# Kernel optimization log

Measured on AMD Instinct MI355X. Metric: run time of the kernel, lower is better.

The kernel has to match this reference:

```python
import jax, jax.numpy as jnp
import numpy as np

D_MODEL = 1280
N_HEADS = 16
DEPTH = D_MODEL // N_HEADS  # 80
NEG_BIG = -10000.0


def setup_inputs() -> dict:
    key = jax.random.key(0)
    ks = jax.random.split(key, 12)
    B, S = 2, 2048
    std = 1.0 / np.sqrt(D_MODEL)
    inp = {
        "v": jax.random.normal(ks[0], (B, S, D_MODEL), jnp.float32),
        "k": jax.random.normal(ks[1], (B, S, D_MODEL), jnp.float32),
        "q": jax.random.normal(ks[2], (B, S, D_MODEL), jnp.float32),
        # causal mask: 1.0 on strictly-upper triangle (future positions)
        "mask": jnp.triu(jnp.ones((S, S), jnp.float32), k=1),
        "Wq_w": jax.random.normal(ks[3], (D_MODEL, D_MODEL), jnp.float32) * std,
        "Wq_b": jnp.zeros((D_MODEL,), jnp.float32),
        "Wk_w": jax.random.normal(ks[4], (D_MODEL, D_MODEL), jnp.float32) * std,
        "Wk_b": jnp.zeros((D_MODEL,), jnp.float32),
        "Wv_w": jax.random.normal(ks[5], (D_MODEL, D_MODEL), jnp.float32) * std,
        "Wv_b": jnp.zeros((D_MODEL,), jnp.float32),
        "dense_w": jax.random.normal(ks[6], (D_MODEL, D_MODEL), jnp.float32) * std,
        "dense_b": jnp.zeros((D_MODEL,), jnp.float32),
    }
    return inp


def _split_heads(x, B):
    # [B, S, D] -> [B, H, S, depth]
    return x.reshape(B, -1, N_HEADS, DEPTH).transpose(0, 2, 1, 3)


def reference(v, k, q, mask, Wq_w, Wq_b, Wk_w, Wk_b, Wv_w, Wv_b, dense_w, dense_b):
    B = q.shape[0]
    # torch Linear: y = x @ W.T + b
    qh = _split_heads(q @ Wq_w.T + Wq_b, B)
    kh = _split_heads(k @ Wk_w.T + Wk_b, B)
    vh = _split_heads(v @ Wv_w.T + Wv_b, B)

    scale = 1.0 / np.sqrt(DEPTH)
    logits = jnp.einsum("bhqd,bhkd->bhqk", qh, kh) * scale  # [B,H,S,S]
    nd, ns = logits.shape[-2], logits.shape[-1]
    logits = logits + mask[ns - nd:ns, :ns] * NEG_BIG
    attn = jax.nn.softmax(logits, axis=-1)
    out = jnp.einsum("bhqk,bhkd->bhqd", attn, vh)  # [B,H,S,depth]
    out = out.transpose(0, 2, 1, 3).reshape(B, -1, D_MODEL)
    out = out @ dense_w.T + dense_b
    return out, attn
```

## Files before the change

### kernel.cpp

```cpp
#include <hip/hip_runtime.h>
#include <hip/hip_bf16.h>

typedef short frag8 __attribute__((ext_vector_type(8)));
typedef float facc4 __attribute__((ext_vector_type(4)));
typedef float f32x4 __attribute__((ext_vector_type(4)));
typedef unsigned short ushort_t;
typedef unsigned int uint_t;

#define DEV static __device__ __forceinline__

DEV ushort_t f2bf(float f) {
  uint_t u = __float_as_uint(f);
  u += 0x7fffu + ((u >> 16) & 1u);
  return (ushort_t)(u >> 16);
}
DEV uint_t cvt_pk(float lo, float hi) {
  uint_t r;
  asm("v_cvt_pk_bf16_f32 %0, %1, %2" : "=v"(r) : "v"(lo), "v"(hi));
  return r;
}
DEV frag8 pack8(float4 a, float4 b) {
  union { frag8 f; uint4 u; } u_;
  u_.u.x = cvt_pk(a.x, a.y); u_.u.y = cvt_pk(a.z, a.w);
  u_.u.z = cvt_pk(b.x, b.y); u_.u.w = cvt_pk(b.z, b.w);
  return u_.f;
}
DEV void bar_lds() { asm volatile("s_waitcnt lgkmcnt(0)\n\ts_barrier" ::: "memory"); }

constexpr int B_ = 2, S_ = 2048, H_ = 16, DM = 1280, DH = 80, DP = 96;
constexpr size_t IN_E = (size_t)B_ * S_ * DM;
constexpr size_t WT_E = (size_t)DM * DM;
constexpr size_t OFF_WQ = 0;
constexpr size_t OFF_WK = OFF_WQ + WT_E;
constexpr size_t OFF_WV = OFF_WK + WT_E;
constexpr size_t OFF_WD = OFF_WV + WT_E;
constexpr size_t QH_E  = (size_t)B_ * H_ * S_ * DP;
constexpr size_t OFF_QH = OFF_WD + WT_E;
constexpr size_t OFF_KH = OFF_QH + QH_E;
constexpr size_t VT_E  = (size_t)B_ * H_ * DH * S_;
constexpr size_t OFF_VT = OFF_KH + QH_E;
constexpr size_t OFF_OH = OFF_VT + VT_E;

constexpr float QSCALE = 0.16129822f;

__global__ void convert_kernel(const float* __restrict__ wq, const float* __restrict__ wk,
                               const float* __restrict__ wv, const float* __restrict__ wd,
                               ushort_t* __restrict__ ws) {
  size_t i = (size_t)blockIdx.x * blockDim.x + threadIdx.x;
  size_t stride = (size_t)gridDim.x * blockDim.x;
  constexpr size_t TOTAL = 4 * WT_E / 8;
  constexpr size_t NROW = (size_t)B_ * H_ * S_;
  constexpr size_t PADC = 2 * NROW * 2;
  for (size_t c = i; c < TOTAL + PADC; c += stride) {
    if (c < TOTAL) {
      size_t e = c * 8;
      const float* s2; size_t lo;
      if      (e < WT_E)     { s2 = wq; lo = e; }
      else if (e < 2 * WT_E) { s2 = wk; lo = e - WT_E; }
      else if (e < 3 * WT_E) { s2 = wv; lo = e - 2 * WT_E; }
      else                   { s2 = wd; lo = e - 3 * WT_E; }
      float4 a = *(const float4*)(s2 + lo);
      float4 b = *(const float4*)(s2 + lo + 4);
      uint4 o;
      o.x = (uint_t)f2bf(a.x) | ((uint_t)f2bf(a.y) << 16);
      o.y = (uint_t)f2bf(a.z) | ((uint_t)f2bf(a.w) << 16);
      o.z = (uint_t)f2bf(b.x) | ((uint_t)f2bf(b.y) << 16);
      o.w = (uint_t)f2bf(b.z) | ((uint_t)f2bf(b.w) << 16);
      *(uint4*)(ws + e) = o;
    } else {
      size_t rr = c - TOTAL;
      size_t row = rr >> 1;
      size_t base = (row < NROW ? OFF_QH : OFF_KH) + (row & (NROW - 1)) * DP + DH + (rr & 1) * 8;
      uint4 z = {0u, 0u, 0u, 0u};
      *(uint4*)(ws + base) = z;
    }
  }
}

__global__ __launch_bounds__(256) void qkv_kernel(const float* __restrict__ Aq,
                                                  const float* __restrict__ Ak,
                                                  const float* __restrict__ Av,
                                                  const ushort_t* __restrict__ wts,
                                                  const float* __restrict__ bq,
                                                  const float* __restrict__ bk,
                                                  const float* __restrict__ bv,
                                                  ushort_t* __restrict__ qh_o,
                                                  ushort_t* __restrict__ kh_o,
                                                  ushort_t* __restrict__ vt_o) {
  __shared__ __align__(16) ushort_t sA[2][128][40];
  __shared__ __align__(16) ushort_t sB[2][128][40];
  int which = blockIdx.x / 320;
  int local = blockIdx.x - which * 320;
  int swz = (local & 7) * 40 + (local >> 3);
  int tm = swz / 10, tn = swz % 10;
  int m0 = tm * 128, n0 = tn * 128;
  const float* A = which == 0 ? Aq : which == 1 ? Ak : Av;
  const ushort_t* W = wts + (size_t)which * WT_E;
  const float* bias = which == 0 ? bq : which == 1 ? bk : bv;
  int tid = threadIdx.x, l = tid & 63, wv = tid >> 6;
  int lm = l & 15, lg = l >> 4;
  int wr = wv >> 1, wc = wv & 1;
  int srow = tid >> 2, schk = tid & 3;
  facc4 acc[4][4] = {};
  frag8 ra[2], rb[2];

  auto load_tile = [&](int kt) {
    const float* Ab = A + (size_t)(m0 + srow) * DM + kt * 32 + schk * 8;
    ra[0] = pack8(*(const float4*)Ab, *(const float4*)(Ab + 4));
    const float* Ab2 = Ab + (size_t)64 * DM;
    ra[1] = pack8(*(const float4*)Ab2, *(const float4*)(Ab2 + 4));
    const ushort_t* Bb = W + (size_t)(n0 + srow) * DM + kt * 32 + schk * 8;
    rb[0] = *(const frag8*)Bb;
    rb[1] = *(const frag8*)(Bb + (size_t)64 * DM);
  };
  auto store_tile = [&](int bb) {
    *(frag8*)&sA[bb][srow][schk * 8] = ra[0];
    *(frag8*)&sA[bb][srow + 64][schk * 8] = ra[1];
    *(frag8*)&sB[bb][srow][schk * 8] = rb[0];
    *(frag8*)&sB[bb][srow + 64][schk * 8] = rb[1];
  };

  load_tile(0);
  store_tile(0);
  __syncthreads();
  for (int kt = 0; kt < 40; ++kt) {
    int cur = kt & 1;
    if (kt < 39) load_tile(kt + 1);
    frag8 af[4], bf[4];
#pragma unroll
    for (int i = 0; i < 4; ++i) af[i] = *(const frag8*)&sA[cur][wr * 64 + i * 16 + lm][lg * 8];
#pragma unroll
    for (int i = 0; i < 4; ++i) bf[i] = *(const frag8*)&sB[cur][wc * 64 + i * 16 + lm][lg * 8];
#pragma unroll
    for (int mi = 0; mi < 4; ++mi)
#pragma unroll
      for (int ni = 0; ni < 4; ++ni)
        acc[mi][ni] = __builtin_amdgcn_mfma_f32_16x16x32_bf16(af[mi], bf[ni], acc[mi][ni], 0, 0, 0);
    if (kt < 39) store_tile(cur ^ 1);
    __syncthreads();
  }

  float scale = (which == 0) ? QSCALE : 1.0f;
  ushort_t* dst = which == 0 ? qh_o : which == 1 ? kh_o : vt_o;
#pragma unroll
  for (int ni = 0; ni < 4; ++ni) {
    int n = n0 + wc * 64 + ni * 16 + lm;
    float bv2 = bias[n];
    int h = n / 80, d = n % 80;
#pragma unroll
    for (int mi = 0; mi < 4; ++mi) {
      int mbase = m0 + wr * 64 + mi * 16 + lg * 4;
      int b = mbase >> 11, sp = mbase & 2047;
      if (which < 2) {
#pragma unroll
        for (int r = 0; r < 4; ++r) {
          float vl = (acc[mi][ni][r] + bv2) * scale;
          dst[((size_t)(b * H_ + h) * S_ + sp + r) * DP + d] = f2bf(vl);
        }
      } else {
        uint2 u2;
        u2.x = cvt_pk(acc[mi][ni][0] + bv2, acc[mi][ni][1] + bv2);
        u2.y = cvt_pk(acc[mi][ni][2] + bv2, acc[mi][ni][3] + bv2);
        *(uint2*)&dst[((size_t)(b * H_ + h) * DH + d) * S_ + sp] = u2;
      }
    }
  }
}

__global__ __launch_bounds__(256) void dense_kernel(const ushort_t* __restrict__ A,
                                                    const ushort_t* __restrict__ W,
                                                    const float* __restrict__ bias,
                                                    float* __restrict__ dst_f) {
  __shared__ __align__(16) ushort_t sA[2][128][40];
  __shared__ __align__(16) ushort_t sB[2][128][40];
  int bid = blockIdx.x;
  int swz = (bid & 7) * 40 + (bid >> 3);
  int tm = swz / 10, tn = swz % 10;
  int m0 = tm * 128, n0 = tn * 128;
  int tid = threadIdx.x, l = tid & 63, wv = tid >> 6;
  int lm = l & 15, lg = l >> 4;
  int wr = wv >> 1, wc = wv & 1;
  int srow = tid >> 2, schk = tid & 3;
  facc4 acc[4][4] = {};
  frag8 ra[2], rb[2];

  auto load_tile = [&](int kt) {
    const ushort_t* Ab = A + (size_t)(m0 + srow) * DM + kt * 32 + schk * 8;
    ra[0] = *(const frag8*)Ab;
    ra[1] = *(const frag8*)(Ab + (size_t)64 * DM);
    const ushort_t* Bb = W + (size_t)(n0 + srow) * DM + kt * 32 + schk * 8;
    rb[0] = *(const frag8*)Bb;
    rb[1] = *(const frag8*)(Bb + (size_t)64 * DM);
  };
  auto store_tile = [&](int bb) {
    *(frag8*)&sA[bb][srow][schk * 8] = ra[0];
    *(frag8*)&sA[bb][srow + 64][schk * 8] = ra[1];
    *(frag8*)&sB[bb][srow][schk * 8] = rb[0];
    *(frag8*)&sB[bb][srow + 64][schk * 8] = rb[1];
  };

  load_tile(0);
  store_tile(0);
  __syncthreads();
  for (int kt = 0; kt < 40; ++kt) {
    int cur = kt & 1;
    if (kt < 39) load_tile(kt + 1);
    frag8 af[4], bf[4];
#pragma unroll
    for (int i = 0; i < 4; ++i) af[i] = *(const frag8*)&sA[cur][wr * 64 + i * 16 + lm][lg * 8];
#pragma unroll
    for (int i = 0; i < 4; ++i) bf[i] = *(const frag8*)&sB[cur][wc * 64 + i * 16 + lm][lg * 8];
#pragma unroll
    for (int mi = 0; mi < 4; ++mi)
#pragma unroll
      for (int ni = 0; ni < 4; ++ni)
        acc[mi][ni] = __builtin_amdgcn_mfma_f32_16x16x32_bf16(af[mi], bf[ni], acc[mi][ni], 0, 0, 0);
    if (kt < 39) store_tile(cur ^ 1);
    __syncthreads();
  }

#pragma unroll
  for (int ni = 0; ni < 4; ++ni) {
    int n = n0 + wc * 64 + ni * 16 + lm;
    float bv2 = bias[n];
#pragma unroll
    for (int mi = 0; mi < 4; ++mi) {
      int mbase = m0 + wr * 64 + mi * 16 + lg * 4;
#pragma unroll
      for (int r = 0; r < 4; ++r)
        __builtin_nontemporal_store(acc[mi][ni][r] + bv2, dst_f + (size_t)(mbase + r) * DM + n);
    }
  }
}

__global__ __launch_bounds__(512, 4) void attn_kernel(const ushort_t* __restrict__ qh,
                                                      const ushort_t* __restrict__ kh,
                                                      const ushort_t* __restrict__ vt,
                                                      ushort_t* __restrict__ outh,
                                                      float* __restrict__ out_attn) {
  __shared__ __align__(16) ushort_t sK[2][64][104];
  __shared__ __align__(16) ushort_t sV[2][80][68];
  __shared__ __align__(16) char sP[8 * 2048];
  int bid = blockIdx.x;
  int half = bid >> 8, rr0 = bid & 255;
  int swz = (rr0 & 7) * 32 + (rr0 >> 3);
  int bh = swz >> 3, pr = swz & 7;
  int b = bh >> 4, h = bh & 15;
  int s = half ? (15 - pr) : pr;
  int tid = threadIdx.x, w = tid >> 6, l = tid & 63, lm = l & 15, lg = l >> 4;
  const ushort_t* qhb = qh + (size_t)bh * S_ * DP;
  const ushort_t* khb = kh + (size_t)bh * S_ * DP;
  const ushort_t* vtb = vt + (size_t)bh * DH * S_;
  float* attnb = out_attn + (size_t)bh * S_ * S_;
  char* Pw = sP + w * 2048;

  int sr[3], sc[3];
#pragma unroll
  for (int i = 0; i < 3; ++i) {
    int c = tid * 3 + i;
    sr[i] = c / 24; sc[i] = (c % 24) * 4;
  }
  uint2 stk[3];
  auto ldtK = [&](int t) {
#pragma unroll
    for (int i = 0; i < 3; ++i)
      stk[i] = *(const uint2*)(khb + (size_t)(t * 64 + sr[i]) * DP + sc[i]);
  };
  auto sttK = [&](int bb) {
#pragma unroll
    for (int i = 0; i < 3; ++i)
      *(uint2*)&sK[bb][sr[i]][sc[i]] = stk[i];
  };
  int vrow = tid >> 3, vcol = (tid & 7) * 8;
  uint4 stv0, stv1;
  auto ldtV = [&](int t) {
    stv0 = *(const uint4*)(vtb + (size_t)vrow * S_ + t * 64 + vcol);
    if (tid < 128) stv1 = *(const uint4*)(vtb + (size_t)(64 + vrow) * S_ + t * 64 + vcol);
  };
  auto sttV = [&](int bb) {
    *(uint4*)&sV[bb][vrow][vcol] = stv0;
    if (tid < 128) *(uint4*)&sV[bb][64 + vrow][vcol] = stv1;
  };

  int q0 = s * 128;
  int wq0 = q0 + w * 16;
  int qg = wq0 + lm;

  frag8 qf[3];
#pragma unroll
  for (int kd = 0; kd < 3; ++kd)
    qf[kd] = *(const frag8*)(qhb + (size_t)qg * DP + kd * 32 + lg * 8);
  int NT = 2 * (s + 1);

  float rs4[4] = {0.f, 0.f, 0.f, 0.f};
  ldtK(0); sttK(0);
  if (NT > 1) ldtK(1);
  bar_lds();
  for (int t = 0; t < NT; ++t) {
    int cur = t & 1;
    if (t + 1 < NT) sttK(cur ^ 1);
    if (t + 2 < NT) ldtK(t + 2);
    if (64 * t < wq0 + 16) {
      facc4 acc[4] = {};
#pragma unroll
      for (int mi = 0; mi < 4; ++mi)
#pragma unroll
        for (int kd = 0; kd < 3; ++kd) {
          frag8 af = *(const frag8*)((const char*)sK + cur * (64 * 104 * 2) +
                                     (mi * 16 + lm) * 208 + kd * 64 + lg * 16);
          acc[mi] = __builtin_amdgcn_mfma_f32_16x16x32_bf16(af, qf[kd], acc[mi], 0, 0, 0);
        }
      if (64 * t + 63 <= wq0) {
#pragma unroll
        for (int mi = 0; mi < 4; ++mi)
#pragma unroll
          for (int r = 0; r < 4; ++r) rs4[r] += exp2f(acc[mi][r]);
      } else {
#pragma unroll
        for (int mi = 0; mi < 4; ++mi)
#pragma unroll
          for (int r = 0; r < 4; ++r) {
            int kg = t * 64 + mi * 16 + lg * 4 + r;
            if (kg <= qg) rs4[r] += exp2f(acc[mi][r]);
          }
      }
    }
    bar_lds();
  }
  float rs = (rs4[0] + rs4[1]) + (rs4[2] + rs4[3]);
  rs += __shfl_xor(rs, 16);
  rs += __shfl_xor(rs, 32);
  float li = -__log2f(rs);

  facc4 acc2[5] = {};
  ldtK(0); ldtV(0); sttK(0); sttV(0);
  if (NT > 1) { ldtK(1); ldtV(1); }
  bar_lds();
  for (int t = 0; t < NT; ++t) {
    int cur = t & 1;
    if (t + 1 < NT) { sttK(cur ^ 1); sttV(cur ^ 1); }
    if (t + 2 < NT) { ldtK(t + 2); ldtV(t + 2); }
    if (64 * t >= wq0 + 16) {
      f32x4 z = {0.f, 0.f, 0.f, 0.f};
#pragma unroll
      for (int mi = 0; mi < 4; ++mi)
        *(f32x4*)(attnb + (size_t)qg * S_ + t * 64 + mi * 16 + lg * 4) = z;
    } else {
      facc4 acc[4] = {};
#pragma unroll
      for (int mi = 0; mi < 4; ++mi)
#pragma unroll
        for (int kd = 0; kd < 3; ++kd) {
          frag8 af = *(const frag8*)((const char*)sK + cur * (64 * 104 * 2) +
                                     (mi * 16 + lm) * 208 + kd * 64 + lg * 16);
          acc[mi] = __builtin_amdgcn_mfma_f32_16x16x32_bf16(af, qf[kd], acc[mi], 0, 0, 0);
        }
      bool full = (64 * t + 63 <= wq0);
#pragma unroll
      for (int mi = 0; mi < 4; ++mi) {
        float p[4];
        if (full) {
#pragma unroll
          for (int r = 0; r < 4; ++r) p[r] = exp2f(acc[mi][r] + li);
        } else {
#pragma unroll
          for (int r = 0; r < 4; ++r) {
            int kg = t * 64 + mi * 16 + lg * 4 + r;
            p[r] = (kg <= qg) ? exp2f(acc[mi][r] + li) : 0.f;
          }
        }
        f32x4 f4 = {p[0], p[1], p[2], p[3]};
        *(f32x4*)(attnb + (size_t)qg * S_ + t * 64 + mi * 16 + lg * 4) = f4;
        uint2 pk;
        pk.x = cvt_pk(p[0], p[1]);
        pk.y = cvt_pk(p[2], p[3]);
        int kb = mi * 32 + lg * 8;
        *(uint2*)(Pw + lm * 128 + (kb ^ ((lm & 7) << 4))) = pk;
      }
#pragma unroll
      for (int ks = 0; ks < 2; ++ks) {
        int kbyte = ks * 64 + lg * 16;
        frag8 pa = *(const frag8*)(Pw + lm * 128 + (kbyte ^ ((lm & 7) << 4)));
#pragma unroll
        for (int nf = 0; nf < 5; ++nf) {
          frag8 vb = *(const frag8*)&sV[cur][nf * 16 + lm][ks * 32 + lg * 8];
          acc2[nf] = __builtin_amdgcn_mfma_f32_16x16x32_bf16(pa, vb, acc2[nf], 0, 0, 0);
        }
      }
    }
    bar_lds();
  }
#pragma unroll
  for (int nf = 0; nf < 5; ++nf)
#pragma unroll
    for (int r = 0; r < 4; ++r) {
      int qrow = q0 + w * 16 + lg * 4 + r;
      int col = h * DH + nf * 16 + lm;
      outh[((size_t)b * S_ + qrow) * DM + col] = f2bf(acc2[nf][r]);
    }

  if (s < 15) {
    int c0 = (s + 1) * 128;
    int r2 = tid >> 2;
    int l4 = (tid & 3) << 2;
    float* rowp = attnb + (size_t)(q0 + r2) * S_ + c0 + l4;
    f32x4 z = {0.f, 0.f, 0.f, 0.f};
    for (int cc = 0; cc < 2048 - c0; cc += 16)
      __builtin_nontemporal_store(z, (f32x4*)(rowp + cc));
  }
}

extern "C" void kernel_launch(void* const* d_in, const int* in_sizes, int n_in,
                              void* d_out, int out_size, void* d_ws, size_t ws_size,
                              hipStream_t stream) {
  const float* v  = (const float*)d_in[0];
  const float* k  = (const float*)d_in[1];
  const float* q  = (const float*)d_in[2];
  const float* wq = (const float*)d_in[4];
  const float* bq = (const float*)d_in[5];
  const float* wk = (const float*)d_in[6];
  const float* bk = (const float*)d_in[7];
  const float* wv = (const float*)d_in[8];
  const float* bv = (const float*)d_in[9];
  const float* wd = (const float*)d_in[10];
  const float* bd = (const float*)d_in[11];
  ushort_t* ws = (ushort_t*)d_ws;
  float* out  = (float*)d_out;
  float* attn = out + IN_E;

  convert_kernel<<<2048, 256, 0, stream>>>(wq, wk, wv, wd, ws);
  qkv_kernel<<<960, 256, 0, stream>>>(q, k, v, ws + OFF_WQ, bq, bk, bv,
                                      ws + OFF_QH, ws + OFF_KH, ws + OFF_VT);
  attn_kernel<<<512, 512, 0, stream>>>(ws + OFF_QH, ws + OFF_KH, ws + OFF_VT, ws + OFF_OH, attn);
  dense_kernel<<<320, 256, 0, stream>>>(ws + OFF_OH, ws + OFF_WD, bd, out);
}
```

Before: 318.9 us.

## Split softmax row-sum pass into separate kernel parallelized over key halves

Moves the first attention pass, which computes the softmax denominators, out of attn_kernel into a new sweep1_kernel. That kernel splits each query block's key range into two halves across twice as many blocks, has a lighter LDS footprint allowing higher occupancy, and combines the partial sums with atomicAdd into a zeroed workspace buffer. attn_kernel then reads the precomputed sums and runs only the second pass. The aim is better parallelism and occupancy for the row-sum pass. The cost is an extra launch, a workspace zeroing step, atomics, and reading K twice across kernels.

New measurement: 347.0 us. 8.8% more time.

```diff
diff --git a/kernel.cpp b/kernel.cpp
--- a/kernel.cpp
+++ b/kernel.cpp
@@ -40,6 +40,7 @@
 constexpr size_t VT_E  = (size_t)B_ * H_ * DH * S_;
 constexpr size_t OFF_VT = OFF_KH + QH_E;
 constexpr size_t OFF_OH = OFF_VT + VT_E;
+constexpr size_t OFF_LS = OFF_OH + IN_E;
 
 constexpr float QSCALE = 0.16129822f;
 
@@ -51,7 +52,8 @@
   constexpr size_t TOTAL = 4 * WT_E / 8;
   constexpr size_t NROW = (size_t)B_ * H_ * S_;
   constexpr size_t PADC = 2 * NROW * 2;
-  for (size_t c = i; c < TOTAL + PADC; c += stride) {
+  constexpr size_t LSC  = 131072 / 8;
+  for (size_t c = i; c < TOTAL + PADC + LSC; c += stride) {
     if (c < TOTAL) {
       size_t e = c * 8;
       const float* s2; size_t lo;
@@ -67,12 +69,16 @@
       o.z = (uint_t)f2bf(b.x) | ((uint_t)f2bf(b.y) << 16);
       o.w = (uint_t)f2bf(b.z) | ((uint_t)f2bf(b.w) << 16);
       *(uint4*)(ws + e) = o;
-    } else {
+    } else if (c < TOTAL + PADC) {
       size_t rr = c - TOTAL;
       size_t row = rr >> 1;
       size_t base = (row < NROW ? OFF_QH : OFF_KH) + (row & (NROW - 1)) * DP + DH + (rr & 1) * 8;
       uint4 z = {0u, 0u, 0u, 0u};
       *(uint4*)(ws + base) = z;
+    } else {
+      size_t idx = c - TOTAL - PADC;
+      uint4 z = {0u, 0u, 0u, 0u};
+      *(uint4*)(ws + OFF_LS + idx * 8) = z;
     }
   }
 }
@@ -233,9 +239,96 @@
   }
 }
 
+__global__ __launch_bounds__(512, 8) void sweep1_kernel(const ushort_t* __restrict__ qh,
+                                                        const ushort_t* __restrict__ kh,
+                                                        float* __restrict__ lsum) {
+  __shared__ __align__(16) ushort_t sK[2][64][104];
+  int bid = blockIdx.x;
+  int khalf = bid >> 9;
+  int rr9 = bid & 511;
+  int half = rr9 >> 8, rr0 = rr9 & 255;
+  int swz = (rr0 & 7) * 32 + (rr0 >> 3);
+  int bh = swz >> 3, pr = swz & 7;
+  int s = half ? (15 - pr) : pr;
+  int tid = threadIdx.x, w = tid >> 6, l = tid & 63, lm = l & 15, lg = l >> 4;
+  const ushort_t* qhb = qh + (size_t)bh * S_ * DP;
+  const ushort_t* khb = kh + (size_t)bh * S_ * DP;
+
+  int sr[3], sc[3];
+#pragma unroll
+  for (int i = 0; i < 3; ++i) {
+    int c = tid * 3 + i;
+    sr[i] = c / 24; sc[i] = (c % 24) * 4;
+  }
+  uint2 stk[3];
+  auto ldtK = [&](int t) {
+#pragma unroll
+    for (int i = 0; i < 3; ++i)
+      stk[i] = *(const uint2*)(khb + (size_t)(t * 64 + sr[i]) * DP + sc[i]);
+  };
+  auto sttK = [&](int bb) {
+#pragma unroll
+    for (int i = 0; i < 3; ++i)
+      *(uint2*)&sK[bb][sr[i]][sc[i]] = stk[i];
+  };
+
+  int q0 = s * 128;
+  int wq0 = q0 + w * 16;
+  int qg = wq0 + lm;
+
+  frag8 qf[3];
+#pragma unroll
+  for (int kd = 0; kd < 3; ++kd)
+    qf[kd] = *(const frag8*)(qhb + (size_t)qg * DP + kd * 32 + lg * 8);
+  int ntile = s + 1;
+  int t0 = khalf * ntile;
+
+  float rs4[4] = {0.f, 0.f, 0.f, 0.f};
+  ldtK(t0); sttK(0);
+  if (ntile > 1) ldtK(t0 + 1);
+  bar_lds();
+  for (int tt = 0; tt < ntile; ++tt) {
+    int t = t0 + tt;
+    int cur = tt & 1;
+    if (tt + 1 < ntile) sttK(cur ^ 1);
+    if (tt + 2 < ntile) ldtK(t0 + tt + 2);
+    if (64 * t < wq0 + 16) {
+      facc4 acc[4] = {};
+#pragma unroll
+      for (int mi = 0; mi < 4; ++mi)
+#pragma unroll
+        for (int kd = 0; kd < 3; ++kd) {
+          frag8 af = *(const frag8*)((const char*)sK + cur * (64 * 104 * 2) +
+                                     (mi * 16 + lm) * 208 + kd * 64 + lg * 16);
+          acc[mi] = __builtin_amdgcn_mfma_f32_16x16x32_bf16(af, qf[kd], acc[mi], 0, 0, 0);
+        }
+      if (64 * t + 63 <= wq0) {
+#pragma unroll
+        for (int mi = 0; mi < 4; ++mi)
+#pragma unroll
+          for (int r = 0; r < 4; ++r) rs4[r] += exp2f(acc[mi][r]);
+      } else {
+#pragma unroll
+        for (int mi = 0; mi < 4; ++mi)
+#pragma unroll
+          for (int r = 0; r < 4; ++r) {
+            int kg = t * 64 + mi * 16 + lg * 4 + r;
+            if (kg <= qg) rs4[r] += exp2f(acc[mi][r]);
+          }
+      }
+    }
+    bar_lds();
+  }
+  float rs = (rs4[0] + rs4[1]) + (rs4[2] + rs4[3]);
+  rs += __shfl_xor(rs, 16);
+  rs += __shfl_xor(rs, 32);
+  if (l < 16) atomicAdd(&lsum[(size_t)bh * S_ + qg], rs);
+}
+
 __global__ __launch_bounds__(512, 4) void attn_kernel(const ushort_t* __restrict__ qh,
                                                       const ushort_t* __restrict__ kh,
                                                       const ushort_t* __restrict__ vt,
+                                                      const float* __restrict__ lsum,
                                                       ushort_t* __restrict__ outh,
                                                       float* __restrict__ out_attn) {
   __shared__ __align__(16) ushort_t sK[2][64][104];
@@ -291,46 +384,7 @@
   for (int kd = 0; kd < 3; ++kd)
     qf[kd] = *(const frag8*)(qhb + (size_t)qg * DP + kd * 32 + lg * 8);
   int NT = 2 * (s + 1);
-
-  float rs4[4] = {0.f, 0.f, 0.f, 0.f};
-  ldtK(0); sttK(0);
-  if (NT > 1) ldtK(1);
-  bar_lds();
-  for (int t = 0; t < NT; ++t) {
-    int cur = t & 1;
-    if (t + 1 < NT) sttK(cur ^ 1);
-    if (t + 2 < NT) ldtK(t + 2);
-    if (64 * t < wq0 + 16) {
-      facc4 acc[4] = {};
-#pragma unroll
-      for (int mi = 0; mi < 4; ++mi)
-#pragma unroll
-        for (int kd = 0; kd < 3; ++kd) {
-          frag8 af = *(const frag8*)((const char*)sK + cur * (64 * 104 * 2) +
-                                     (mi * 16 + lm) * 208 + kd * 64 + lg * 16);
-          acc[mi] = __builtin_amdgcn_mfma_f32_16x16x32_bf16(af, qf[kd], acc[mi], 0, 0, 0);
-        }
-      if (64 * t + 63 <= wq0) {
-#pragma unroll
-        for (int mi = 0; mi < 4; ++mi)
-#pragma unroll
-          for (int r = 0; r < 4; ++r) rs4[r] += exp2f(acc[mi][r]);
-      } else {
-#pragma unroll
-        for (int mi = 0; mi < 4; ++mi)
-#pragma unroll
-          for (int r = 0; r < 4; ++r) {
-            int kg = t * 64 + mi * 16 + lg * 4 + r;
-            if (kg <= qg) rs4[r] += exp2f(acc[mi][r]);
-          }
-      }
-    }
-    bar_lds();
-  }
-  float rs = (rs4[0] + rs4[1]) + (rs4[2] + rs4[3]);
-  rs += __shfl_xor(rs, 16);
-  rs += __shfl_xor(rs, 32);
-  float li = -__log2f(rs);
+  float li = -__log2f(lsum[(size_t)bh * S_ + qg]);
 
   facc4 acc2[5] = {};
   ldtK(0); ldtV(0); sttK(0); sttV(0);
@@ -425,12 +479,15 @@
   const float* wd = (const float*)d_in[10];
   const float* bd = (const float*)d_in[11];
   ushort_t* ws = (ushort_t*)d_ws;
+  float* lsum = (float*)(ws + OFF_LS);
   float* out  = (float*)d_out;
   float* attn = out + IN_E;
 
   convert_kernel<<<2048, 256, 0, stream>>>(wq, wk, wv, wd, ws);
   qkv_kernel<<<960, 256, 0, stream>>>(q, k, v, ws + OFF_WQ, bq, bk, bv,
                                       ws + OFF_QH, ws + OFF_KH, ws + OFF_VT);
-  attn_kernel<<<512, 512, 0, stream>>>(ws + OFF_QH, ws + OFF_KH, ws + OFF_VT, ws + OFF_OH, attn);
+  sweep1_kernel<<<1024, 512, 0, stream>>>(ws + OFF_QH, ws + OFF_KH, lsum);
+  attn_kernel<<<512, 512, 0, stream>>>(ws + OFF_QH, ws + OFF_KH, ws + OFF_VT, lsum,
+                                       ws + OFF_OH, attn);
   dense_kernel<<<320, 256, 0, stream>>>(ws + OFF_OH, ws + OFF_WD, bd, out);
 }
```
